# Kernel optimization log

Hardware: AMD Instinct MI355X
Metric: run time of the kernel (lower is better)

The kernel has to match this reference:

```python
import jax, jax.numpy as jnp
import numpy as np

CONV_K = 4
C_EXP = 8.0  # Griffin exponent constant
EPS = 1.1920929e-07  # torch RMSNorm default eps = finfo(float32).eps


def rmsnorm(x, w):
    return x * jax.lax.rsqrt(jnp.mean(x * x, axis=-1, keepdims=True) + EPS) * w


def gelu(x):
    return jax.nn.gelu(x, approximate=False)  # torch F.gelu default (erf)


def setup_inputs() -> dict:
    B, T, D = 16, 1024, 1024
    H = 4 * D  # GatedMLP hidden
    key = jax.random.key(0)
    ks = jax.random.split(key, 16)
    s = 0.02
    return {
        "x_seq": jax.random.normal(ks[0], (B, T, D), jnp.float32),
        "h0": jnp.zeros((B, D), jnp.float32),
        "conv_buf": jax.random.normal(ks[1], (B, CONV_K - 1, D), jnp.float32),
        "norm1_w": jnp.ones((D,), jnp.float32),
        "W1": jax.random.normal(ks[2], (D, D), jnp.float32) * s,
        "conv_w": jax.random.normal(ks[3], (D, CONV_K), jnp.float32) * s,
        "conv_b": jnp.zeros((D,), jnp.float32),
        "Wa": jax.random.normal(ks[4], (D, D), jnp.float32) * s,
        "ba": jnp.zeros((D,), jnp.float32),
        "Wx": jax.random.normal(ks[5], (D, D), jnp.float32) * s,
        "bx": jnp.zeros((D,), jnp.float32),
        "log_lambda": jnp.linspace(0.0, 4.0, D).astype(jnp.float32),
        "W2": jax.random.normal(ks[6], (D, D), jnp.float32) * s,
        "Wout": jax.random.normal(ks[7], (D, D), jnp.float32) * s,
        "norm2_w": jnp.ones((D,), jnp.float32),
        "Wg": jax.random.normal(ks[8], (H, D), jnp.float32) * s,
        "Wu": jax.random.normal(ks[9], (H, D), jnp.float32) * s,
        "Wo": jax.random.normal(ks[10], (D, H), jnp.float32) * s,
    }


def _block(x_seq, h0, conv_buf, norm1_w, W1, conv_w, conv_b, Wa, ba, Wx, bx,
           log_lambda, W2, Wout, norm2_w, Wg, Wu, Wo):
    B, T, D = x_seq.shape
    normed = rmsnorm(x_seq, norm1_w)
    b1 = normed @ W1.T                                   # (B,T,D)
    padded = jnp.concatenate([conv_buf, b1], axis=1)     # (B,T+3,D)
    # depthwise causal conv (cross-correlation, matching torch Conv1d)
    b1_conv = conv_b
    for k in range(CONV_K):
        b1_conv = b1_conv + padded[:, k:k + T, :] * conv_w[:, k]
    new_conv_buf = padded[:, -(CONV_K - 1):, :]

    # RG-LRU: precompute gates, scan only the diagonal linear recurrence
    r = jax.nn.sigmoid(b1_conv @ Wa.T + ba)
    i = jax.nn.sigmoid(b1_conv @ Wx.T + bx)
    a = jnp.exp((C_EXP * r) * jax.nn.log_sigmoid(log_lambda))  # sigmoid(L)**(c*r)
    gate = jnp.sqrt(jnp.clip((1.0 - a) * (1.0 + a), 1e-06))
    u = gate * (i * b1_conv)

    def step(h, au):
        a_t, u_t = au
        h = a_t * h + u_t
        return h, h

    new_h, outs = jax.lax.scan(step, h0,
                               (jnp.swapaxes(a, 0, 1), jnp.swapaxes(u, 0, 1)))
    b1_out = jnp.swapaxes(outs, 0, 1)                    # (B,T,D)

    b2 = gelu(normed @ W2.T)
    recurrent_out = (b1_out * b2) @ Wout.T
    x1 = x_seq + recurrent_out

    n2 = rmsnorm(x1, norm2_w)
    mlp = (gelu(n2 @ Wg.T) * (n2 @ Wu.T)) @ Wo.T         # GeGLU gated MLP
    x2 = x1 + mlp
    return x2, new_h, new_conv_buf


def reference(x_seq, h0, conv_buf, norm1_w, W1, conv_w, conv_b, Wa, ba, Wx, bx,
              log_lambda, W2, Wout, norm2_w, Wg, Wu, Wo):
    return _block(x_seq, h0, conv_buf, norm1_w, W1, conv_w, conv_b, Wa, ba,
                  Wx, bx, log_lambda, W2, Wout, norm2_w, Wg, Wu, Wo)
```

## Files before the change

kernel.cpp:

```cpp
#include <hip/hip_runtime.h>
#include <hip/hip_bf16.h>
#include <cstdint>

using bf16 = __hip_bfloat16;
typedef __attribute__((ext_vector_type(8))) short bf16x8;
typedef __attribute__((ext_vector_type(4))) float f32x4;

#define NB 16
#define NT_ 1024
#define ND 1024
#define NH 4096
#define NM (NB * NT_)

enum { EPI_BF16 = 0, EPI_OM, EPI_U, EPI_GELU, EPI_GELU_MUL, EPI_X1, EPI_X2 };

__device__ __forceinline__ float sigm(float x) { return 1.0f / (1.0f + expf(-x)); }
__device__ __forceinline__ float gelu_f(float x) { return 0.5f * x * (1.0f + erff(x * 0.7071067811865476f)); }
__device__ __forceinline__ float b2f(bf16 h) { return __bfloat162float(h); }
__device__ __forceinline__ bf16  f2b(float x) { return __float2bfloat16(x); }

__device__ __forceinline__ void gl_lds16(const bf16* g, void* l) {
  __builtin_amdgcn_global_load_lds((const __attribute__((address_space(1))) void*)g,
                                   (__attribute__((address_space(3))) void*)l, 16, 0, 0);
}

template <int EPI>
__global__ __launch_bounds__(512, 2)
void gemm256(const bf16* __restrict__ A, const bf16* __restrict__ Bw,
             int M, int N, int K,
             const float* __restrict__ biasf, const float* __restrict__ vecf,
             const bf16* __restrict__ auxb, const bf16* __restrict__ auxb2,
             const float* __restrict__ auxf,
             float* __restrict__ outf, bf16* __restrict__ outb)
{
  (void)M;
  __shared__ __align__(16) bf16x8 lds8[8192];
  const int tid  = (int)threadIdx.x;
  const int wave = tid >> 6, lane = tid & 63;
  const int lr = lane & 15, lq = lane >> 4;
  const int wm = wave >> 2, wn = wave & 3;

  const int nwg = (int)gridDim.x;
  const int swz = ((int)blockIdx.x & 7) * (nwg >> 3) + ((int)blockIdx.x >> 3);
  const int nbx = N >> 8;
  const int by = swz / nbx, bx = swz - by * nbx;
  const int m0 = by << 8, n0 = bx << 8;
  const int NT = K >> 5;

  const bf16* __restrict__ Ag = A  + (long)m0 * K;
  const bf16* __restrict__ Bg = Bw + (long)n0 * K;

  const int lrow = lane >> 2;
  const int kbs  = (lane & 3) ^ (((lane >> 5) & 1) << 1);
  const int lqs = lq ^ ((lr & 8) >> 2);
  const int lr4lqs = lr * 4 + lqs;
  const int aRd = wm * 512 + lr4lqs;
  const int bRd = 1024 + wn * 256 + lr4lqs;

  const bf16 *gA0, *gA1, *gB0, *gB1;
  int dA0, dA1;
  {
    const int cc0 = wave * 2, cc1 = wave * 2 + 1;
    const int kc = kbs * 8;
    gA0 = Ag + (long)(cc0 * 16 + lrow) * K + kc;
    gA1 = Ag + (long)(cc1 * 16 + lrow) * K + kc;
    gB0 = Bg + (long)(cc0 * 16 + lrow) * K + kc;
    gB1 = Bg + (long)(cc1 * 16 + lrow) * K + kc;
    dA0 = cc0 * 1024 + lane * 16;
    dA1 = cc1 * 1024 + lane * 16;
  }

#define STAGE(BUFIDX) do { \
    char* Lb_ = ((char*)lds8) + (BUFIDX) * 32768; \
    gl_lds16(gA0, Lb_ + dA0);          gl_lds16(gA1, Lb_ + dA1); \
    gl_lds16(gB0, Lb_ + 16384 + dA0);  gl_lds16(gB1, Lb_ + 16384 + dA1); \
    gA0 += 32; gA1 += 32; gB0 += 32; gB1 += 32; } while (0)

  f32x4 acc[8][4];
#pragma unroll
  for (int i = 0; i < 8; ++i)
#pragma unroll
    for (int jj = 0; jj < 4; ++jj)
#pragma unroll
      for (int r = 0; r < 4; ++r) acc[i][jj][r] = 0.0f;

  STAGE(0);
  STAGE(1);

#define KTILE(T, BUF) do { \
    if ((T) + 2 < NT) { \
      STAGE(((BUF) + 2) & 3); \
      asm volatile("s_waitcnt vmcnt(8)" ::: "memory"); \
    } else if ((T) + 1 < NT) { \
      asm volatile("s_waitcnt vmcnt(4)" ::: "memory"); \
    } else { \
      asm volatile("s_waitcnt vmcnt(0)" ::: "memory"); \
    } \
    asm volatile("s_barrier" ::: "memory"); \
    const int cb_ = (BUF) * 2048; \
    bf16x8 bF[4]; \
    _Pragma("unroll") for (int j_ = 0; j_ < 4; ++j_) \
      bF[j_] = lds8[cb_ + bRd + j_ * 64]; \
    _Pragma("unroll") for (int i_ = 0; i_ < 8; ++i_) { \
      bf16x8 a_ = lds8[cb_ + aRd + i_ * 64]; \
      _Pragma("unroll") for (int j_ = 0; j_ < 4; ++j_) \
        acc[i_][j_] = __builtin_amdgcn_mfma_f32_16x16x32_bf16(a_, bF[j_], acc[i_][j_], 0, 0, 0); \
    } \
  } while (0)

  for (int t = 0; t < NT; t += 4) {
    KTILE(t + 0, 0);
    KTILE(t + 1, 1);
    KTILE(t + 2, 2);
    KTILE(t + 3, 3);
  }
#undef KTILE
#undef STAGE

  const int col0 = n0 + wn * 64 + lr;
  float bj[4], vj[4];
  if constexpr (EPI == EPI_OM || EPI == EPI_U) {
#pragma unroll
    for (int j = 0; j < 4; ++j) bj[j] = biasf[col0 + j * 16];
  }
  if constexpr (EPI == EPI_OM) {
#pragma unroll
    for (int j = 0; j < 4; ++j) vj[j] = -log1pf(expf(-vecf[col0 + j * 16]));
  }
  const long NL = (long)N, N12 = 12 * NL;
  long er = (long)(m0 + wm * 128 + lq * 4) * NL + col0;
#pragma unroll
  for (int i = 0; i < 8; ++i) {
#pragma unroll
    for (int r = 0; r < 4; ++r) {
#pragma unroll
      for (int j = 0; j < 4; ++j) {
        const long idx = er + j * 16;
        float v = acc[i][j][r];
        if constexpr (EPI == EPI_BF16) {
          outb[idx] = f2b(v);
        } else if constexpr (EPI == EPI_OM) {
          float rr = sigm(v + bj[j]);
          outb[idx] = f2b(-expm1f(8.0f * rr * vj[j]));
        } else if constexpr (EPI == EPI_U) {
          float ii = sigm(v + bj[j]);
          float om = b2f(auxb2[idx]);
          float g  = sqrtf(fmaxf(om * (2.0f - om), 1e-6f));
          outb[idx] = f2b(g * ii * b2f(auxb[idx]));
        } else if constexpr (EPI == EPI_GELU) {
          outb[idx] = f2b(gelu_f(v));
        } else if constexpr (EPI == EPI_GELU_MUL) {
          float u2 = b2f(outb[idx]);
          outb[idx] = f2b(gelu_f(v) * u2);
        } else if constexpr (EPI == EPI_X1) {
          outb[idx] = f2b(v + auxf[idx]);
        } else if constexpr (EPI == EPI_X2) {
          outf[idx] = v + b2f(auxb[idx]);
        }
      }
      er += NL;
    }
    er += N12;
  }
}

__global__ __launch_bounds__(256)
void cast4_kernel(const float* __restrict__ in, bf16* __restrict__ out, long n4) {
  long i = (long)blockIdx.x * 256 + threadIdx.x;
  if (i < n4) {
    float4 v = reinterpret_cast<const float4*>(in)[i];
    union { bf16 h[4]; ushort4 u; } pk;
    pk.h[0] = f2b(v.x); pk.h[1] = f2b(v.y); pk.h[2] = f2b(v.z); pk.h[3] = f2b(v.w);
    reinterpret_cast<ushort4*>(out)[i] = pk.u;
  }
}

template <typename TIN>
__global__ __launch_bounds__(256)
void rmsnorm_kernel(const TIN* __restrict__ x, const float* __restrict__ w,
                    bf16* __restrict__ out) {
  const int row = blockIdx.x;
  const int t = threadIdx.x;
  float4 v;
  if constexpr (sizeof(TIN) == 4) {
    v = reinterpret_cast<const float4*>(x + (long)row * ND)[t];
  } else {
    union { ushort4 u; bf16 h[4]; } xv;
    xv.u = reinterpret_cast<const ushort4*>(x + (long)row * ND)[t];
    v = make_float4(b2f(xv.h[0]), b2f(xv.h[1]), b2f(xv.h[2]), b2f(xv.h[3]));
  }
  float ss = v.x * v.x + v.y * v.y + v.z * v.z + v.w * v.w;
#pragma unroll
  for (int off = 32; off > 0; off >>= 1) ss += __shfl_down(ss, off, 64);
  __shared__ float red[4];
  if ((t & 63) == 0) red[t >> 6] = ss;
  __syncthreads();
  float tot = red[0] + red[1] + red[2] + red[3];
  float scale = rsqrtf(tot * (1.0f / ND) + 1.1920929e-07f);
  float4 wv = reinterpret_cast<const float4*>(w)[t];
  union { bf16 h[4]; ushort4 u; } pk;
  pk.h[0] = f2b(v.x * scale * wv.x);
  pk.h[1] = f2b(v.y * scale * wv.y);
  pk.h[2] = f2b(v.z * scale * wv.z);
  pk.h[3] = f2b(v.w * scale * wv.w);
  reinterpret_cast<ushort4*>(out + (long)row * ND)[t] = pk.u;
}

__global__ __launch_bounds__(256)
void conv_kernel(const bf16* __restrict__ b1, const float* __restrict__ conv_buf,
                 const float* __restrict__ conv_w, const float* __restrict__ conv_b,
                 bf16* __restrict__ out_b1c, float* __restrict__ out_newbuf) {
  const long gid = (long)blockIdx.x * 256 + threadIdx.x;
  const int d = (int)(gid & (ND - 1));
  const long bt = gid >> 10;
  const int t = (int)(bt & (NT_ - 1));
  const int b = (int)(bt >> 10);
  float acc = conv_b[d];
#pragma unroll
  for (int k = 0; k < 4; ++k) {
    const int p = t + k;
    float src = (p < 3) ? conv_buf[((long)b * 3 + p) * ND + d]
                        : b2f(b1[((long)b * NT_ + (p - 3)) * ND + d]);
    acc = fmaf(conv_w[d * 4 + k], src, acc);
  }
  out_b1c[gid] = f2b(acc);
  if (t >= NT_ - 3)
    out_newbuf[((long)b * 3 + (t - (NT_ - 3))) * ND + d] = b2f(b1[gid]);
}

__global__ __launch_bounds__(256)
void scan_kernel(const bf16* __restrict__ om, const bf16* __restrict__ u,
                 const bf16* __restrict__ b2, const float* __restrict__ h0,
                 bf16* __restrict__ prod, float* __restrict__ newh) {
  const int gid = blockIdx.x * 256 + threadIdx.x;
  const int d = gid & (ND - 1);
  const int b = gid >> 10;
  float h = h0[gid];
  const long base = (long)b * NT_ * ND + d;
#pragma unroll 8
  for (int t = 0; t < NT_; ++t) {
    const long idx = base + (long)t * ND;
    h = fmaf(-b2f(om[idx]), h, h) + b2f(u[idx]);
    prod[idx] = f2b(h * b2f(b2[idx]));
  }
  newh[gid] = h;
}

extern "C" void kernel_launch(void* const* d_in, const int* in_sizes, int n_in,
                              void* d_out, int out_size, void* d_ws, size_t ws_size,
                              hipStream_t stream) {
  const float* x_seq    = (const float*)d_in[0];
  const float* h0       = (const float*)d_in[1];
  const float* conv_buf = (const float*)d_in[2];
  const float* norm1_w  = (const float*)d_in[3];
  const float* W1       = (const float*)d_in[4];
  const float* conv_w   = (const float*)d_in[5];
  const float* conv_b   = (const float*)d_in[6];
  const float* Wa       = (const float*)d_in[7];
  const float* ba       = (const float*)d_in[8];
  const float* Wx       = (const float*)d_in[9];
  const float* bx       = (const float*)d_in[10];
  const float* loglam   = (const float*)d_in[11];
  const float* W2       = (const float*)d_in[12];
  const float* Wout     = (const float*)d_in[13];
  const float* norm2_w  = (const float*)d_in[14];
  const float* Wg       = (const float*)d_in[15];
  const float* Wu       = (const float*)d_in[16];
  const float* Wo       = (const float*)d_in[17];

  char* ws = (char*)d_ws;
  bf16* normed = (bf16*)(ws);
  bf16* b1buf  = (bf16*)(ws + (32L  << 20));
  bf16* b1cbuf = (bf16*)(ws + (64L  << 20));
  bf16* Woutb  = (bf16*)(ws + (64L  << 20));
  bf16* ombuf  = (bf16*)(ws + (96L  << 20));
  bf16* ubuf   = (bf16*)(ws + (128L << 20));
  bf16* x1buf  = (bf16*)(ws + (160L << 20));
  bf16* b2buf  = x1buf;
  bf16* bigbuf = (bf16*)(ws + (32L  << 20));
  bf16* W1b    = (bf16*)(ws + (192L << 20));
  bf16* Wab    = (bf16*)(ws + (194L << 20));
  bf16* Wxb    = (bf16*)(ws + (196L << 20));
  bf16* W2b    = (bf16*)(ws + (198L << 20));
  bf16* Wgb    = (bf16*)(ws + (200L << 20));
  bf16* Wub    = (bf16*)(ws + (208L << 20));
  bf16* Wob    = (bf16*)(ws + (216L << 20));

  float* out_x2 = (float*)d_out;
  float* out_h  = out_x2 + (long)NM * ND;
  float* out_cb = out_h + NB * ND;

  const dim3 blk(256);
  const dim3 blk512(512);
  const dim3 gD256((NM / 256) * (ND / 256));
  const dim3 gH256((NM / 256) * (NH / 256));

  cast4_kernel<<<dim3(1024), blk, 0, stream>>>(W1, W1b, 262144);
  cast4_kernel<<<dim3(1024), blk, 0, stream>>>(Wa, Wab, 262144);
  cast4_kernel<<<dim3(1024), blk, 0, stream>>>(Wx, Wxb, 262144);
  cast4_kernel<<<dim3(1024), blk, 0, stream>>>(W2, W2b, 262144);
  cast4_kernel<<<dim3(4096), blk, 0, stream>>>(Wg, Wgb, 1048576);
  cast4_kernel<<<dim3(4096), blk, 0, stream>>>(Wu, Wub, 1048576);
  cast4_kernel<<<dim3(4096), blk, 0, stream>>>(Wo, Wob, 1048576);

  rmsnorm_kernel<float><<<dim3(NM), blk, 0, stream>>>(x_seq, norm1_w, normed);
  gemm256<EPI_BF16><<<gD256, blk512, 0, stream>>>(normed, W1b, NM, ND, ND,
      nullptr, nullptr, nullptr, nullptr, nullptr, nullptr, b1buf);
  conv_kernel<<<dim3((NM * ND) / 256), blk, 0, stream>>>(b1buf, conv_buf, conv_w, conv_b,
      b1cbuf, out_cb);
  gemm256<EPI_OM><<<gD256, blk512, 0, stream>>>(b1cbuf, Wab, NM, ND, ND,
      ba, loglam, nullptr, nullptr, nullptr, nullptr, ombuf);
  gemm256<EPI_U><<<gD256, blk512, 0, stream>>>(b1cbuf, Wxb, NM, ND, ND,
      bx, nullptr, b1cbuf, ombuf, nullptr, nullptr, ubuf);
  gemm256<EPI_GELU><<<gD256, blk512, 0, stream>>>(normed, W2b, NM, ND, ND,
      nullptr, nullptr, nullptr, nullptr, nullptr, nullptr, b2buf);
  scan_kernel<<<dim3(NB * ND / 256), blk, 0, stream>>>(ombuf, ubuf, b2buf, h0, b1buf, out_h);
  cast4_kernel<<<dim3(1024), blk, 0, stream>>>(Wout, Woutb, 262144);
  gemm256<EPI_X1><<<gD256, blk512, 0, stream>>>(b1buf, Woutb, NM, ND, ND,
      nullptr, nullptr, nullptr, nullptr, x_seq, nullptr, x1buf);
  rmsnorm_kernel<bf16><<<dim3(NM), blk, 0, stream>>>(x1buf, norm2_w, normed);
  gemm256<EPI_BF16><<<gH256, blk512, 0, stream>>>(normed, Wub, NM, NH, ND,
      nullptr, nullptr, nullptr, nullptr, nullptr, nullptr, bigbuf);
  gemm256<EPI_GELU_MUL><<<gH256, blk512, 0, stream>>>(normed, Wgb, NM, NH, ND,
      nullptr, nullptr, nullptr, nullptr, nullptr, nullptr, bigbuf);
  gemm256<EPI_X2><<<gD256, blk512, 0, stream>>>(bigbuf, Wob, NM, ND, NH,
      nullptr, nullptr, x1buf, nullptr, nullptr, out_x2, nullptr);
}
```

Measured before the change: 1.148 ms.

## Shrink GEMM tiles to 128x128 with 256 threads and double buffering

Replaces the 256x256-tile, 512-thread GEMM that used a 4-deep LDS ring with fine-grained vmcnt waits by a 128x128-tile, 256-thread kernel. The new kernel uses a 2-buffer LDS pipeline with __syncthreads after each k-tile. The aim is higher occupancy and more workgroups in flight. The cost is halved data reuse per tile, more global and LDS traffic, and a shallower prefetch with full barriers, which may expose load latency.

```diff
diff --git a/kernel.cpp b/kernel.cpp
--- a/kernel.cpp
+++ b/kernel.cpp
@@ -25,8 +25,8 @@
 }
 
 template <int EPI>
-__global__ __launch_bounds__(512, 2)
-void gemm256(const bf16* __restrict__ A, const bf16* __restrict__ Bw,
+__global__ __launch_bounds__(256, 4)
+void gemm128(const bf16* __restrict__ A, const bf16* __restrict__ Bw,
              int M, int N, int K,
              const float* __restrict__ biasf, const float* __restrict__ vecf,
              const bf16* __restrict__ auxb, const bf16* __restrict__ auxb2,
@@ -34,17 +34,17 @@
              float* __restrict__ outf, bf16* __restrict__ outb)
 {
   (void)M;
-  __shared__ __align__(16) bf16x8 lds8[8192];
+  __shared__ __align__(16) bf16x8 lds8[2048];
   const int tid  = (int)threadIdx.x;
   const int wave = tid >> 6, lane = tid & 63;
   const int lr = lane & 15, lq = lane >> 4;
-  const int wm = wave >> 2, wn = wave & 3;
+  const int wm = wave >> 1, wn = wave & 1;
 
   const int nwg = (int)gridDim.x;
   const int swz = ((int)blockIdx.x & 7) * (nwg >> 3) + ((int)blockIdx.x >> 3);
-  const int nbx = N >> 8;
+  const int nbx = N >> 7;
   const int by = swz / nbx, bx = swz - by * nbx;
-  const int m0 = by << 8, n0 = bx << 8;
+  const int m0 = by << 7, n0 = bx << 7;
   const int NT = K >> 5;
 
   const bf16* __restrict__ Ag = A  + (long)m0 * K;
@@ -53,9 +53,8 @@
   const int lrow = lane >> 2;
   const int kbs  = (lane & 3) ^ (((lane >> 5) & 1) << 1);
   const int lqs = lq ^ ((lr & 8) >> 2);
-  const int lr4lqs = lr * 4 + lqs;
-  const int aRd = wm * 512 + lr4lqs;
-  const int bRd = 1024 + wn * 256 + lr4lqs;
+  const int aRd = wm * 256 + lr * 4 + lqs;
+  const int bRd = 512 + wn * 256 + lr * 4 + lqs;
 
   const bf16 *gA0, *gA1, *gB0, *gB1;
   int dA0, dA1;
@@ -70,51 +69,42 @@
     dA1 = cc1 * 1024 + lane * 16;
   }
 
-#define STAGE(BUFIDX) do { \
-    char* Lb_ = ((char*)lds8) + (BUFIDX) * 32768; \
-    gl_lds16(gA0, Lb_ + dA0);          gl_lds16(gA1, Lb_ + dA1); \
-    gl_lds16(gB0, Lb_ + 16384 + dA0);  gl_lds16(gB1, Lb_ + 16384 + dA1); \
+#define STAGE(BUF) do { \
+    char* Lb_ = ((char*)lds8) + (BUF) * 16384; \
+    gl_lds16(gA0, Lb_ + dA0);         gl_lds16(gA1, Lb_ + dA1); \
+    gl_lds16(gB0, Lb_ + 8192 + dA0);  gl_lds16(gB1, Lb_ + 8192 + dA1); \
     gA0 += 32; gA1 += 32; gB0 += 32; gB1 += 32; } while (0)
 
-  f32x4 acc[8][4];
-#pragma unroll
-  for (int i = 0; i < 8; ++i)
+  f32x4 acc[4][4];
+#pragma unroll
+  for (int i = 0; i < 4; ++i)
 #pragma unroll
     for (int jj = 0; jj < 4; ++jj)
 #pragma unroll
       for (int r = 0; r < 4; ++r) acc[i][jj][r] = 0.0f;
 
   STAGE(0);
-  STAGE(1);
-
-#define KTILE(T, BUF) do { \
-    if ((T) + 2 < NT) { \
-      STAGE(((BUF) + 2) & 3); \
-      asm volatile("s_waitcnt vmcnt(8)" ::: "memory"); \
-    } else if ((T) + 1 < NT) { \
-      asm volatile("s_waitcnt vmcnt(4)" ::: "memory"); \
-    } else { \
-      asm volatile("s_waitcnt vmcnt(0)" ::: "memory"); \
-    } \
-    asm volatile("s_barrier" ::: "memory"); \
-    const int cb_ = (BUF) * 2048; \
+  __syncthreads();
+
+#define TILE2(T, CUR) do { \
+    if ((T) + 1 < NT) STAGE((CUR) ^ 1); \
+    const int cb_ = (CUR) * 1024; \
     bf16x8 bF[4]; \
     _Pragma("unroll") for (int j_ = 0; j_ < 4; ++j_) \
       bF[j_] = lds8[cb_ + bRd + j_ * 64]; \
-    _Pragma("unroll") for (int i_ = 0; i_ < 8; ++i_) { \
+    _Pragma("unroll") for (int i_ = 0; i_ < 4; ++i_) { \
       bf16x8 a_ = lds8[cb_ + aRd + i_ * 64]; \
       _Pragma("unroll") for (int j_ = 0; j_ < 4; ++j_) \
         acc[i_][j_] = __builtin_amdgcn_mfma_f32_16x16x32_bf16(a_, bF[j_], acc[i_][j_], 0, 0, 0); \
     } \
+    __syncthreads(); \
   } while (0)
 
-  for (int t = 0; t < NT; t += 4) {
-    KTILE(t + 0, 0);
-    KTILE(t + 1, 1);
-    KTILE(t + 2, 2);
-    KTILE(t + 3, 3);
-  }
-#undef KTILE
+  for (int t = 0; t < NT; t += 2) {
+    TILE2(t, 0);
+    TILE2(t + 1, 1);
+  }
+#undef TILE2
 #undef STAGE
 
   const int col0 = n0 + wn * 64 + lr;
@@ -128,9 +118,9 @@
     for (int j = 0; j < 4; ++j) vj[j] = -log1pf(expf(-vecf[col0 + j * 16]));
   }
   const long NL = (long)N, N12 = 12 * NL;
-  long er = (long)(m0 + wm * 128 + lq * 4) * NL + col0;
-#pragma unroll
-  for (int i = 0; i < 8; ++i) {
+  long er = (long)(m0 + wm * 64 + lq * 4) * NL + col0;
+#pragma unroll
+  for (int i = 0; i < 4; ++i) {
 #pragma unroll
     for (int r = 0; r < 4; ++r) {
 #pragma unroll
@@ -291,9 +281,8 @@
   float* out_cb = out_h + NB * ND;
 
   const dim3 blk(256);
-  const dim3 blk512(512);
-  const dim3 gD256((NM / 256) * (ND / 256));
-  const dim3 gH256((NM / 256) * (NH / 256));
+  const dim3 gD128((NM / 128) * (ND / 128));
+  const dim3 gH128((NM / 128) * (NH / 128));
 
   cast4_kernel<<<dim3(1024), blk, 0, stream>>>(W1, W1b, 262144);
   cast4_kernel<<<dim3(1024), blk, 0, stream>>>(Wa, Wab, 262144);
@@ -304,25 +293,25 @@
   cast4_kernel<<<dim3(4096), blk, 0, stream>>>(Wo, Wob, 1048576);
 
   rmsnorm_kernel<float><<<dim3(NM), blk, 0, stream>>>(x_seq, norm1_w, normed);
-  gemm256<EPI_BF16><<<gD256, blk512, 0, stream>>>(normed, W1b, NM, ND, ND,
+  gemm128<EPI_BF16><<<gD128, blk, 0, stream>>>(normed, W1b, NM, ND, ND,
       nullptr, nullptr, nullptr, nullptr, nullptr, nullptr, b1buf);
   conv_kernel<<<dim3((NM * ND) / 256), blk, 0, stream>>>(b1buf, conv_buf, conv_w, conv_b,
       b1cbuf, out_cb);
-  gemm256<EPI_OM><<<gD256, blk512, 0, stream>>>(b1cbuf, Wab, NM, ND, ND,
+  gemm128<EPI_OM><<<gD128, blk, 0, stream>>>(b1cbuf, Wab, NM, ND, ND,
       ba, loglam, nullptr, nullptr, nullptr, nullptr, ombuf);
-  gemm256<EPI_U><<<gD256, blk512, 0, stream>>>(b1cbuf, Wxb, NM, ND, ND,
+  gemm128<EPI_U><<<gD128, blk, 0, stream>>>(b1cbuf, Wxb, NM, ND, ND,
       bx, nullptr, b1cbuf, ombuf, nullptr, nullptr, ubuf);
-  gemm256<EPI_GELU><<<gD256, blk512, 0, stream>>>(normed, W2b, NM, ND, ND,
+  gemm128<EPI_GELU><<<gD128, blk, 0, stream>>>(normed, W2b, NM, ND, ND,
       nullptr, nullptr, nullptr, nullptr, nullptr, nullptr, b2buf);
   scan_kernel<<<dim3(NB * ND / 256), blk, 0, stream>>>(ombuf, ubuf, b2buf, h0, b1buf, out_h);
   cast4_kernel<<<dim3(1024), blk, 0, stream>>>(Wout, Woutb, 262144);
-  gemm256<EPI_X1><<<gD256, blk512, 0, stream>>>(b1buf, Woutb, NM, ND, ND,
+  gemm128<EPI_X1><<<gD128, blk, 0, stream>>>(b1buf, Woutb, NM, ND, ND,
       nullptr, nullptr, nullptr, nullptr, x_seq, nullptr, x1buf);
   rmsnorm_kernel<bf16><<<dim3(NM), blk, 0, stream>>>(x1buf, norm2_w, normed);
-  gemm256<EPI_BF16><<<gH256, blk512, 0, stream>>>(normed, Wub, NM, NH, ND,
+  gemm128<EPI_BF16><<<gH128, blk, 0, stream>>>(normed, Wub, NM, NH, ND,
       nullptr, nullptr, nullptr, nullptr, nullptr, nullptr, bigbuf);
-  gemm256<EPI_GELU_MUL><<<gH256, blk512, 0, stream>>>(normed, Wgb, NM, NH, ND,
+  gemm128<EPI_GELU_MUL><<<gH128, blk, 0, stream>>>(normed, Wgb, NM, NH, ND,
       nullptr, nullptr, nullptr, nullptr, nullptr, nullptr, bigbuf);
-  gemm256<EPI_X2><<<gD256, blk512, 0, stream>>>(bigbuf, Wob, NM, ND, NH,
+  gemm128<EPI_X2><<<gD128, blk, 0, stream>>>(bigbuf, Wob, NM, ND, NH,
       nullptr, nullptr, x1buf, nullptr, nullptr, out_x2, nullptr);
 }
```

New measurement: 1.177 ms. +2.5%, slower.
